# Performance work log

Hardware: AMD Instinct MI355X
Metric: run time of the kernel (lower is better)

## Reference

```python
import jax, jax.numpy as jnp
import numpy as np
import math

B, S, E, H = 4, 4096, 1024, 64

def setup_inputs() -> dict:
    key = jax.random.key(0)
    ks = jax.random.split(key, 4)
    scale = 1.0 / math.sqrt(E)
    return {
        "x": jax.random.normal(ks[0], (B, S, E), dtype=jnp.float32),
        "Wq": jax.random.normal(ks[1], (E, H), dtype=jnp.float32) * scale,
        "bq": jnp.zeros((H,), dtype=jnp.float32),
        "Wk": jax.random.normal(ks[2], (E, H), dtype=jnp.float32) * scale,
        "bk": jnp.zeros((H,), dtype=jnp.float32),
        "Wv": jax.random.normal(ks[3], (E, H), dtype=jnp.float32) * scale,
        "bv": jnp.zeros((H,), dtype=jnp.float32),
    }

def reference(x, Wq, bq, Wk, bk, Wv, bv):
    # x: [B,S,E]; single-head causal attention with dropout p=0 (eval).
    q = jnp.einsum("bse,eh->bsh", x, Wq) + bq  # [B,S,H]
    k = jnp.einsum("bse,eh->bsh", x, Wk) + bk
    v = jnp.einsum("bse,eh->bsh", x, Wv) + bv
    head_size = q.shape[-1]
    scores = jnp.einsum("bqh,bkh->bqk", q, k)  # [B,S,S]
    causal = jnp.tril(jnp.ones((q.shape[1], k.shape[1]), dtype=bool))
    # original: masked_fill(-inf) then divide by sqrt(head_size) -> same math
    scores = jnp.where(causal, scores, -jnp.inf) / jnp.sqrt(jnp.float32(head_size)).astype(scores.dtype)
    weight = jax.nn.softmax(scores, axis=-1)
    out = jnp.einsum("bqk,bkh->bqh", weight, v)  # [B,S,H]
    return out
```

## Files before the change

### kernel.cpp

```cpp
#include <hip/hip_runtime.h>

#define BATCH 4
#define SEQ   4096
#define EMB   1024
#define HD    64
#define NROW  (BATCH*SEQ)

typedef float f32x4  __attribute__((ext_vector_type(4)));
typedef short bf16x8 __attribute__((ext_vector_type(8)));
typedef short bf16x4 __attribute__((ext_vector_type(4)));

#define LOG2E 1.4426950408889634f
#define EXP2(x) exp2f(x)

static __device__ __forceinline__ f32x4 MFMA16(bf16x4 a, bf16x4 b, f32x4 c) {
#if defined(__HIP_DEVICE_COMPILE__) && __has_builtin(__builtin_amdgcn_mfma_f32_16x16x16bf16_1k)
  return __builtin_amdgcn_mfma_f32_16x16x16bf16_1k(a, b, c, 0, 0, 0);
#elif defined(__HIP_DEVICE_COMPILE__)
  f32x4 d;
  asm volatile("v_mfma_f32_16x16x16_bf16 %0, %1, %2, %3"
               : "=v"(d) : "v"(a), "v"(b), "v"(c));
  return d;
#else
  return c;
#endif
}

static __device__ __forceinline__ short f2bf(float f) {
  union { float f; unsigned u; } v; v.f = f;
  unsigned r = v.u + 0x7fffu + ((v.u >> 16) & 1u);
  return (short)(r >> 16);
}
static __device__ __forceinline__ float bf2f(short s) {
  union { unsigned u; float f; } v; v.u = ((unsigned)(unsigned short)s) << 16;
  return v.f;
}
static __device__ __forceinline__ unsigned cvtpk(float lo, float hi) {
  unsigned r;
  asm("v_cvt_pk_bf16_f32 %0, %1, %2" : "=v"(r) : "v"(lo), "v"(hi));
  return r;
}
static __device__ __forceinline__ float max3f(float a, float b, float c) {
  float r;
  asm("v_max3_f32 %0, %1, %2, %3" : "=v"(r) : "v"(a), "v"(b), "v"(c));
  return r;
}
static __device__ __forceinline__ bf16x4 pack4(unsigned w01, unsigned w23) {
  union { unsigned u[2]; bf16x4 v; } x;
  x.u[0] = w01; x.u[1] = w23;
  return x.v;
}

__global__ __launch_bounds__(256) void wt_kernel(
    const float* __restrict__ Wq, const float* __restrict__ Wk,
    const float* __restrict__ Wv, short* __restrict__ Wtf) {
  __shared__ float t[64][65];
  int bid = blockIdx.x;
  int mat = bid >> 4;
  int et  = bid & 15;
  int e0  = et * 64;
  const float* W = (mat == 0) ? Wq : (mat == 1) ? Wk : Wv;
  int c  = threadIdx.x & 63;
  int r0 = threadIdx.x >> 6;
#pragma unroll
  for (int i = 0; i < 16; ++i)
    t[i * 4 + r0][c] = W[(size_t)(e0 + i * 4 + r0) * HD + c];
  __syncthreads();
#pragma unroll
  for (int half = 0; half < 2; ++half) {
    int cid  = half * 256 + threadIdx.x;
    int ct4  = cid >> 7;
    int ksl  = (cid >> 6) & 1;
    int lane = cid & 63;
    int g    = lane >> 4;
    int mi   = lane & 15;
    int ct   = mat * 4 + ct4;
    int ks   = et * 2 + ksl;
    bf16x8 v;
#pragma unroll
    for (int j = 0; j < 8; ++j)
      v[j] = f2bf(t[ksl * 32 + 8 * g + j][ct4 * 16 + mi]);
    *(bf16x8*)(Wtf + ((size_t)(ct * 32 + ks) * 64 + lane) * 8) = v;
  }
}

__global__ __launch_bounds__(256) void qkv_kernel(
    const float* __restrict__ X, const short* __restrict__ Wtf,
    const float* __restrict__ bq, const float* __restrict__ bk, const float* __restrict__ bv,
    short* __restrict__ Qf, short* __restrict__ Kf, short* __restrict__ Vf) {
  __shared__ __align__(16) short xs[2][2][32][32];
  __shared__ float part[2][12][4][64];

  int tid  = threadIdx.x;
  int w    = tid >> 6;
  int lane = tid & 63;
  int g    = lane >> 4;
  int mi   = lane & 15;
  int rs   = w & 1;
  int h    = w >> 1;
  int rowbase = blockIdx.x * 32;

  int sr = tid >> 3;
  int sc = tid & 7;
  const float* xsrc = X + (size_t)(rowbase + sr) * EMB + sc * 4;

  f32x4 acc[12];
#pragma unroll
  for (int i = 0; i < 12; ++i) acc[i] = (f32x4){0.f, 0.f, 0.f, 0.f};

  {
    float4 xa = *(const float4*)(xsrc);
    float4 xb = *(const float4*)(xsrc + 512);
    bf16x4 va, vb;
    va[0] = f2bf(xa.x); va[1] = f2bf(xa.y); va[2] = f2bf(xa.z); va[3] = f2bf(xa.w);
    vb[0] = f2bf(xb.x); vb[1] = f2bf(xb.y); vb[2] = f2bf(xb.z); vb[3] = f2bf(xb.w);
    *(bf16x4*)(&xs[0][0][sr][sc * 4]) = va;
    *(bf16x4*)(&xs[0][1][sr][sc * 4]) = vb;
  }
  __syncthreads();

  const short* wp = Wtf + (size_t)(h * 16) * 512 + lane * 8;

#pragma unroll 2
  for (int ks = 0; ks < 16; ++ks) {
    int buf = ks & 1;
    float4 xa, xb;
    if (ks < 15) {
      xa = *(const float4*)(xsrc + (ks + 1) * 32);
      xb = *(const float4*)(xsrc + (ks + 1) * 32 + 512);
    }
    bf16x8 af = *(const bf16x8*)(&xs[buf][h][rs * 16 + mi][g * 8]);
    const short* wk = wp + ks * 512;
#pragma unroll
    for (int ct = 0; ct < 12; ++ct) {
      bf16x8 bfr = *(const bf16x8*)(wk + (size_t)ct * 16384);
      acc[ct] = __builtin_amdgcn_mfma_f32_16x16x32_bf16(af, bfr, acc[ct], 0, 0, 0);
    }
    if (ks < 15) {
      bf16x4 va, vb;
      va[0] = f2bf(xa.x); va[1] = f2bf(xa.y); va[2] = f2bf(xa.z); va[3] = f2bf(xa.w);
      vb[0] = f2bf(xb.x); vb[1] = f2bf(xb.y); vb[2] = f2bf(xb.z); vb[3] = f2bf(xb.w);
      *(bf16x4*)(&xs[buf ^ 1][0][sr][sc * 4]) = va;
      *(bf16x4*)(&xs[buf ^ 1][1][sr][sc * 4]) = vb;
    }
    __syncthreads();
  }

  if (h == 1) {
#pragma unroll
    for (int ct = 0; ct < 12; ++ct)
#pragma unroll
      for (int r = 0; r < 4; ++r) part[rs][ct][r][lane] = acc[ct][r];
  }
  __syncthreads();
  if (h == 0) {
#pragma unroll
    for (int ct = 0; ct < 12; ++ct)
#pragma unroll
      for (int r = 0; r < 4; ++r) part[rs][ct][r][lane] += acc[ct][r];
  }
  __syncthreads();

  int b_  = rowbase >> 12;
  int srb = rowbase & (SEQ - 1);

  {
    int tl  = tid >> 7;
    int kh  = (tid >> 6) & 1;
    int ln  = tid & 63;
    int gg  = ln >> 4;
    int mi2 = ln & 15;
    int tgl = (srb >> 4) + tl;
    bf16x8 vq, vk;
#pragma unroll
    for (int j = 0; j < 8; ++j) {
      int hd = kh * 32 + 8 * gg + j;
      int ct = hd >> 4, cc = hd & 15;
      int li = (mi2 >> 2) * 16 + cc;
      int r2 = mi2 & 3;
      vq[j] = f2bf(part[tl][ct][r2][li] + bq[hd]);
      vk[j] = f2bf(part[tl][4 + ct][r2][li] + bk[hd]);
    }
    size_t chunk = ((size_t)(b_ * 256 + tgl) * 2 + kh) * 512 + ln * 8;
    *(bf16x8*)(Qf + chunk) = vq;
    *(bf16x8*)(Kf + chunk) = vk;
  }
  {
    int ht  = tid >> 6;
    int ln  = tid & 63;
    int gg  = ln >> 4;
    int mi2 = ln & 15;
    int c32 = srb >> 5;
    float bias = bv[ht * 16 + mi2];
    bf16x8 vvv;
#pragma unroll
    for (int hl = 0; hl < 2; ++hl)
#pragma unroll
      for (int j = 0; j < 4; ++j)
        vvv[hl * 4 + j] = f2bf(part[hl][8 + ht][j][gg * 16 + mi2] + bias);
    size_t chunk = ((size_t)(b_ * 128 + c32) * 4 + ht) * 512 + ln * 8;
    *(bf16x8*)(Vf + chunk) = vvv;
  }
}

__global__ __launch_bounds__(512, 4) void attn_kernel(
    const short* __restrict__ Qf, const short* __restrict__ Kf,
    const short* __restrict__ Vf, float* __restrict__ out) {
  __shared__ short lds_o[8][64][17];
  __shared__ float lds_m[8][16];
  __shared__ float lds_l[8][16];

  int tid  = threadIdx.x;
  int w    = tid >> 6;
  int lane = tid & 63;
  int g    = lane >> 4;
  int qi   = lane & 15;

  int bid = blockIdx.x;
  int bb  = bid & 3;
  int jj  = (bid >> 3) + (((bid >> 2) & 1) << 6);

  const float K1 = 0.125f * LOG2E;

  for (int ph = 0; ph < 2; ++ph) {
    int t  = ph ? (255 - jj) : jj;
    int q0 = t * 16;
    int row = q0 + qi;

    const short* qp = Qf + ((size_t)(bb * 256 + t) * 2) * 512 + lane * 8;
    bf16x8 qf0 = *(const bf16x8*)(qp);
    bf16x8 qf1 = *(const bf16x8*)(qp + 512);

    int total64 = (t + 4) >> 2;
    int blo = (w * total64) >> 3;
    int bhi = ((w + 1) * total64) >> 3;

    float m2 = -INFINITY, lsum = 0.f;
    f32x4 o[4];
#pragma unroll
    for (int i = 0; i < 4; ++i) o[i] = (f32x4){0.f, 0.f, 0.f, 0.f};

    for (int b = blo; b < bhi; ++b) {
      int kv0 = b * 64;
      const short* kp = Kf + ((size_t)(bb * 256 + 4 * b) * 2) * 512 + lane * 8;
      const short* vp = Vf + ((size_t)(bb * 128 + 2 * b) * 4) * 512 + lane * 8;

      bf16x8 kfa[4], kfb[4];
#pragma unroll
      for (int c = 0; c < 4; ++c) {
        kfa[c] = *(const bf16x8*)(kp + (c * 2) * 512);
        kfb[c] = *(const bf16x8*)(kp + (c * 2 + 1) * 512);
      }
      bf16x8 vv[8];
#pragma unroll
      for (int i = 0; i < 8; ++i) vv[i] = *(const bf16x8*)(vp + i * 512);

      f32x4 z[4];
      __builtin_amdgcn_s_setprio(1);
#pragma unroll
      for (int c = 0; c < 4; ++c) {
        f32x4 zz = (f32x4){0.f, 0.f, 0.f, 0.f};
        zz = __builtin_amdgcn_mfma_f32_16x16x32_bf16(kfa[c], qf0, zz, 0, 0, 0);
        zz = __builtin_amdgcn_mfma_f32_16x16x32_bf16(kfb[c], qf1, zz, 0, 0, 0);
        z[c] = zz;
      }
      __builtin_amdgcn_s_setprio(0);

      if (kv0 + 63 > q0) {
#pragma unroll
        for (int c = 0; c < 4; ++c)
#pragma unroll
          for (int r = 0; r < 4; ++r) {
            int col = kv0 + c * 16 + 4 * g + r;
            z[c][r] = (col <= row) ? z[c][r] : -INFINITY;
          }
      }

      float l1 = max3f(z[0][0], z[0][1], z[0][2]);
      float l2 = max3f(z[0][3], z[1][0], z[1][1]);
      float l3 = max3f(z[1][2], z[1][3], z[2][0]);
      float l4 = max3f(z[2][1], z[2][2], z[2][3]);
      float l5 = max3f(z[3][0], z[3][1], z[3][2]);
      float lmax = fmaxf(max3f(l1, l2, l3), max3f(l4, l5, z[3][3]));
      bool grow = __any(fmaf(lmax, K1, -8.0f) > m2);
      if (grow) {
        float gm = fmaxf(lmax, __shfl_xor(lmax, 16));
        gm = fmaxf(gm, __shfl_xor(gm, 32));
        float m2n = fmaxf(m2, gm * K1);
        float alpha = EXP2(m2 - m2n);
        m2 = m2n;
        lsum *= alpha;
#pragma unroll
        for (int i = 0; i < 4; ++i) {
          o[i][0] *= alpha; o[i][1] *= alpha; o[i][2] *= alpha; o[i][3] *= alpha;
        }
      }

      float ls = 0.f;
      bf16x4 pb[4];
#pragma unroll
      for (int c = 0; c < 4; ++c) {
        float p0 = EXP2(fmaf(z[c][0], K1, -m2));
        float p1 = EXP2(fmaf(z[c][1], K1, -m2));
        float p2 = EXP2(fmaf(z[c][2], K1, -m2));
        float p3 = EXP2(fmaf(z[c][3], K1, -m2));
        ls += (p0 + p1) + (p2 + p3);
        pb[c] = pack4(cvtpk(p0, p1), cvtpk(p2, p3));
      }
      lsum += ls;

      __builtin_amdgcn_s_setprio(1);
#pragma unroll
      for (int c = 0; c < 4; ++c) {
        int h2 = c >> 1;
#pragma unroll
        for (int ht = 0; ht < 4; ++ht) {
          bf16x8 vfull = vv[h2 * 4 + ht];
          bf16x4 va = (c & 1) ? __builtin_shufflevector(vfull, vfull, 4, 5, 6, 7)
                              : __builtin_shufflevector(vfull, vfull, 0, 1, 2, 3);
          o[ht] = MFMA16(va, pb[c], o[ht]);
        }
      }
      __builtin_amdgcn_s_setprio(0);
    }

    lsum += __shfl_xor(lsum, 16);
    lsum += __shfl_xor(lsum, 32);
#pragma unroll
    for (int ht = 0; ht < 4; ++ht)
#pragma unroll
      for (int r = 0; r < 4; ++r)
        lds_o[w][ht * 16 + 4 * g + r][qi] = f2bf(o[ht][r]);
    if (lane < 16) { lds_m[w][lane] = m2; lds_l[w][lane] = lsum; }
    __syncthreads();

    {
      int q  = tid >> 5;
      int c2 = tid & 31;
      int hb = c2 * 2;
      float mm = lds_m[0][q];
#pragma unroll
      for (int wv = 1; wv < 8; ++wv) mm = fmaxf(mm, lds_m[wv][q]);
      float denom = 0.f, a0 = 0.f, a1 = 0.f;
#pragma unroll
      for (int wv = 0; wv < 8; ++wv) {
        float e = EXP2(lds_m[wv][q] - mm);
        denom += lds_l[wv][q] * e;
        a0 += e * bf2f(lds_o[wv][hb][q]);
        a1 += e * bf2f(lds_o[wv][hb + 1][q]);
      }
      float inv = 1.f / denom;
      float2 res = make_float2(a0 * inv, a1 * inv);
      *(float2*)(out + ((size_t)(bb * SEQ + q0 + q)) * HD + hb) = res;
    }
    __syncthreads();
  }
}

extern "C" void kernel_launch(void* const* d_in, const int* in_sizes, int n_in,
                              void* d_out, int out_size, void* d_ws, size_t ws_size,
                              hipStream_t stream) {
  const float* X  = (const float*)d_in[0];
  const float* Wq = (const float*)d_in[1];
  const float* bq = (const float*)d_in[2];
  const float* Wk = (const float*)d_in[3];
  const float* bk = (const float*)d_in[4];
  const float* Wv = (const float*)d_in[5];
  const float* bv = (const float*)d_in[6];
  float* out = (float*)d_out;

  char* ws = (char*)d_ws;
  const size_t SZ = (size_t)NROW * HD * 2;
  short* Qf  = (short*)(ws);
  short* Kf  = (short*)(ws + SZ);
  short* Vf  = (short*)(ws + 2 * SZ);
  short* Wtf = (short*)(ws + 3 * SZ);

  wt_kernel<<<48, 256, 0, stream>>>(Wq, Wk, Wv, Wtf);
  qkv_kernel<<<NROW / 32, 256, 0, stream>>>(X, Wtf, bq, bk, bv, Qf, Kf, Vf);
  attn_kernel<<<BATCH * 128, 512, 0, stream>>>(Qf, Kf, Vf, out);
}
```

Measured before the change: 56.47 us.

## Restructure QKV projection to 16-row blocks with full-K LDS staging

The QKV projection now processes 16 rows per block instead of 32. It loads the whole 16x1024 X tile into LDS as bf16 with an XOR swizzle, then splits the 12 output column tiles across the 4 waves (3 each). This removes the K-split partial-sum reduction and the per-step double-buffered syncs, and doubles the grid to raise parallelism in this memory-bound kernel. In exchange, each block re-reads the full weight matrix, so weight traffic from L2 per output row doubles, and the V output is written as half-chunk 8-byte stores.

Result: slower. 59.52 us (+5.4%).

```diff
diff --git a/kernel.cpp b/kernel.cpp
--- a/kernel.cpp
+++ b/kernel.cpp
@@ -84,122 +84,95 @@
   }
 }
 
-__global__ __launch_bounds__(256) void qkv_kernel(
+__global__ __launch_bounds__(256, 4) void qkv_kernel(
     const float* __restrict__ X, const short* __restrict__ Wtf,
     const float* __restrict__ bq, const float* __restrict__ bk, const float* __restrict__ bv,
     short* __restrict__ Qf, short* __restrict__ Kf, short* __restrict__ Vf) {
-  __shared__ __align__(16) short xs[2][2][32][32];
-  __shared__ float part[2][12][4][64];
+  __shared__ __align__(16) short xs[16384];
 
   int tid  = threadIdx.x;
   int w    = tid >> 6;
   int lane = tid & 63;
-  int g    = lane >> 4;
-  int mi   = lane & 15;
-  int rs   = w & 1;
-  int h    = w >> 1;
-  int rowbase = blockIdx.x * 32;
-
-  int sr = tid >> 3;
-  int sc = tid & 7;
-  const float* xsrc = X + (size_t)(rowbase + sr) * EMB + sc * 4;
-
-  f32x4 acc[12];
-#pragma unroll
-  for (int i = 0; i < 12; ++i) acc[i] = (f32x4){0.f, 0.f, 0.f, 0.f};
+  int rowbase = blockIdx.x * 16;
 
   {
-    float4 xa = *(const float4*)(xsrc);
-    float4 xb = *(const float4*)(xsrc + 512);
-    bf16x4 va, vb;
-    va[0] = f2bf(xa.x); va[1] = f2bf(xa.y); va[2] = f2bf(xa.z); va[3] = f2bf(xa.w);
-    vb[0] = f2bf(xb.x); vb[1] = f2bf(xb.y); vb[2] = f2bf(xb.z); vb[3] = f2bf(xb.w);
-    *(bf16x4*)(&xs[0][0][sr][sc * 4]) = va;
-    *(bf16x4*)(&xs[0][1][sr][sc * 4]) = vb;
+    int row = w * 4 + (lane >> 4);
+    int kb  = (lane & 15) * 4;
+    const float* xrow = X + (size_t)(rowbase + row) * EMB;
+#pragma unroll 4
+    for (int i = 0; i < 16; ++i) {
+      int k = i * 64 + kb;
+      float4 xv = *(const float4*)(xrow + k);
+      bf16x4 v;
+      v[0] = f2bf(xv.x); v[1] = f2bf(xv.y); v[2] = f2bf(xv.z); v[3] = f2bf(xv.w);
+      int ks = k >> 5, gg = (k >> 3) & 3, jh = (k >> 2) & 1;
+      int sidx = ks * 512 + ((((gg * 16 + row) * 8) ^ ((ks & 7) << 3)) + jh * 4);
+      *(bf16x4*)(&xs[sidx]) = v;
+    }
   }
   __syncthreads();
 
-  const short* wp = Wtf + (size_t)(h * 16) * 512 + lane * 8;
-
-#pragma unroll 2
-  for (int ks = 0; ks < 16; ++ks) {
-    int buf = ks & 1;
-    float4 xa, xb;
-    if (ks < 15) {
-      xa = *(const float4*)(xsrc + (ks + 1) * 32);
-      xb = *(const float4*)(xsrc + (ks + 1) * 32 + 512);
-    }
-    bf16x8 af = *(const bf16x8*)(&xs[buf][h][rs * 16 + mi][g * 8]);
-    const short* wk = wp + ks * 512;
-#pragma unroll
-    for (int ct = 0; ct < 12; ++ct) {
-      bf16x8 bfr = *(const bf16x8*)(wk + (size_t)ct * 16384);
-      acc[ct] = __builtin_amdgcn_mfma_f32_16x16x32_bf16(af, bfr, acc[ct], 0, 0, 0);
-    }
-    if (ks < 15) {
-      bf16x4 va, vb;
-      va[0] = f2bf(xa.x); va[1] = f2bf(xa.y); va[2] = f2bf(xa.z); va[3] = f2bf(xa.w);
-      vb[0] = f2bf(xb.x); vb[1] = f2bf(xb.y); vb[2] = f2bf(xb.z); vb[3] = f2bf(xb.w);
-      *(bf16x4*)(&xs[buf ^ 1][0][sr][sc * 4]) = va;
-      *(bf16x4*)(&xs[buf ^ 1][1][sr][sc * 4]) = vb;
-    }
-    __syncthreads();
-  }
-
-  if (h == 1) {
-#pragma unroll
-    for (int ct = 0; ct < 12; ++ct)
-#pragma unroll
-      for (int r = 0; r < 4; ++r) part[rs][ct][r][lane] = acc[ct][r];
+  f32x4 acc[3];
+#pragma unroll
+  for (int i = 0; i < 3; ++i) acc[i] = (f32x4){0.f, 0.f, 0.f, 0.f};
+  const short* wb = Wtf + ((size_t)(w * 3) * 32) * 512 + lane * 8;
+#pragma unroll 4
+  for (int ks = 0; ks < 32; ++ks) {
+    bf16x8 af = *(const bf16x8*)(&xs[ks * 512 + ((lane * 8) ^ ((ks & 7) << 3))]);
+#pragma unroll
+    for (int i = 0; i < 3; ++i) {
+      bf16x8 bfr = *(const bf16x8*)(wb + ((size_t)(i * 32 + ks)) * 512);
+      acc[i] = __builtin_amdgcn_mfma_f32_16x16x32_bf16(af, bfr, acc[i], 0, 0, 0);
+    }
   }
   __syncthreads();
-  if (h == 0) {
-#pragma unroll
-    for (int ct = 0; ct < 12; ++ct)
-#pragma unroll
-      for (int r = 0; r < 4; ++r) part[rs][ct][r][lane] += acc[ct][r];
+
+  float* part = (float*)xs;
+#pragma unroll
+  for (int i = 0; i < 3; ++i) {
+    int ct = w * 3 + i;
+#pragma unroll
+    for (int r = 0; r < 4; ++r) part[(ct * 4 + r) * 64 + lane] = acc[i][r];
   }
   __syncthreads();
 
   int b_  = rowbase >> 12;
   int srb = rowbase & (SEQ - 1);
+  int tgl = srb >> 4;
+  int c32 = srb >> 5;
+  int hl  = (srb >> 4) & 1;
 
   {
-    int tl  = tid >> 7;
+    int qk  = tid >> 7;
     int kh  = (tid >> 6) & 1;
     int ln  = tid & 63;
     int gg  = ln >> 4;
     int mi2 = ln & 15;
-    int tgl = (srb >> 4) + tl;
-    bf16x8 vq, vk;
+    const float* bp = qk ? bk : bq;
+    bf16x8 v;
 #pragma unroll
     for (int j = 0; j < 8; ++j) {
       int hd = kh * 32 + 8 * gg + j;
-      int ct = hd >> 4, cc = hd & 15;
+      int ct = qk * 4 + (hd >> 4);
+      int cc = hd & 15;
       int li = (mi2 >> 2) * 16 + cc;
       int r2 = mi2 & 3;
-      vq[j] = f2bf(part[tl][ct][r2][li] + bq[hd]);
-      vk[j] = f2bf(part[tl][4 + ct][r2][li] + bk[hd]);
+      v[j] = f2bf(part[(ct * 4 + r2) * 64 + li] + bp[hd]);
     }
     size_t chunk = ((size_t)(b_ * 256 + tgl) * 2 + kh) * 512 + ln * 8;
-    *(bf16x8*)(Qf + chunk) = vq;
-    *(bf16x8*)(Kf + chunk) = vk;
+    *(bf16x8*)((qk ? Kf : Qf) + chunk) = v;
   }
   {
     int ht  = tid >> 6;
     int ln  = tid & 63;
     int gg  = ln >> 4;
     int mi2 = ln & 15;
-    int c32 = srb >> 5;
     float bias = bv[ht * 16 + mi2];
-    bf16x8 vvv;
-#pragma unroll
-    for (int hl = 0; hl < 2; ++hl)
-#pragma unroll
-      for (int j = 0; j < 4; ++j)
-        vvv[hl * 4 + j] = f2bf(part[hl][8 + ht][j][gg * 16 + mi2] + bias);
-    size_t chunk = ((size_t)(b_ * 128 + c32) * 4 + ht) * 512 + ln * 8;
-    *(bf16x8*)(Vf + chunk) = vvv;
+    bf16x4 vv;
+#pragma unroll
+    for (int j = 0; j < 4; ++j)
+      vv[j] = f2bf(part[((8 + ht) * 4 + j) * 64 + gg * 16 + mi2] + bias);
+    *(bf16x4*)(Vf + ((size_t)(b_ * 128 + c32) * 4 + ht) * 512 + ln * 8 + hl * 4) = vv;
   }
 }
 
@@ -377,6 +350,6 @@
   short* Wtf = (short*)(ws + 3 * SZ);
 
   wt_kernel<<<48, 256, 0, stream>>>(Wq, Wk, Wv, Wtf);
-  qkv_kernel<<<NROW / 32, 256, 0, stream>>>(X, Wtf, bq, bk, bv, Qf, Kf, Vf);
+  qkv_kernel<<<NROW / 16, 256, 0, stream>>>(X, Wtf, bq, bk, bv, Qf, Kf, Vf);
   attn_kernel<<<BATCH * 128, 512, 0, stream>>>(Qf, Kf, Vf, out);
 }
```

## Process two query tiles per block to reuse K/V loads across 32 rows

Applied to the files above, without the earlier changes.

Each attention block now computes two 16-row query tiles per phase, sharing each loaded K and V tile across both, and the grid is halved to 256 blocks. This is meant to cut redundant K/V global loads and raise MFMA work per load. In exchange it doubles accumulator registers, lowers launch-bounds occupancy to 2, and leaves only one block per CU, reducing latency hiding and load balance.

Result: no change. 56.47 us, median of 3 (-0.0%).

```diff
diff --git a/kernel.cpp b/kernel.cpp
--- a/kernel.cpp
+++ b/kernel.cpp
@@ -203,12 +203,12 @@
   }
 }
 
-__global__ __launch_bounds__(512, 4) void attn_kernel(
+__global__ __launch_bounds__(512, 2) void attn_kernel(
     const short* __restrict__ Qf, const short* __restrict__ Kf,
     const short* __restrict__ Vf, float* __restrict__ out) {
-  __shared__ short lds_o[8][64][17];
-  __shared__ float lds_m[8][16];
-  __shared__ float lds_l[8][16];
+  __shared__ short lds_o[8][2][64][17];
+  __shared__ float lds_m[8][2][16];
+  __shared__ float lds_l[8][2][16];
 
   int tid  = threadIdx.x;
   int w    = tid >> 6;
@@ -218,27 +218,33 @@
 
   int bid = blockIdx.x;
   int bb  = bid & 3;
-  int jj  = (bid >> 3) + (((bid >> 2) & 1) << 6);
+  int j   = bid >> 2;
 
   const float K1 = 0.125f * LOG2E;
 
   for (int ph = 0; ph < 2; ++ph) {
-    int t  = ph ? (255 - jj) : jj;
-    int q0 = t * 16;
-    int row = q0 + qi;
-
-    const short* qp = Qf + ((size_t)(bb * 256 + t) * 2) * 512 + lane * 8;
-    bf16x8 qf0 = *(const bf16x8*)(qp);
-    bf16x8 qf1 = *(const bf16x8*)(qp + 512);
-
-    int total64 = (t + 4) >> 2;
+    int G  = ph ? (127 - j) : j;
+    int q0 = G * 32;
+
+    bf16x8 qf0[2], qf1[2];
+#pragma unroll
+    for (int tl = 0; tl < 2; ++tl) {
+      const short* qp = Qf + ((size_t)(bb * 256 + 2 * G + tl) * 2) * 512 + lane * 8;
+      qf0[tl] = *(const bf16x8*)(qp);
+      qf1[tl] = *(const bf16x8*)(qp + 512);
+    }
+
+    int total64 = (G + 2) >> 1;
     int blo = (w * total64) >> 3;
     int bhi = ((w + 1) * total64) >> 3;
 
-    float m2 = -INFINITY, lsum = 0.f;
-    f32x4 o[4];
-#pragma unroll
-    for (int i = 0; i < 4; ++i) o[i] = (f32x4){0.f, 0.f, 0.f, 0.f};
+    float m2[2]   = {-INFINITY, -INFINITY};
+    float lsum[2] = {0.f, 0.f};
+    f32x4 o[2][4];
+#pragma unroll
+    for (int tl = 0; tl < 2; ++tl)
+#pragma unroll
+      for (int i = 0; i < 4; ++i) o[tl][i] = (f32x4){0.f, 0.f, 0.f, 0.f};
 
     for (int b = blo; b < bhi; ++b) {
       int kv0 = b * 64;
@@ -255,103 +261,119 @@
 #pragma unroll
       for (int i = 0; i < 8; ++i) vv[i] = *(const bf16x8*)(vp + i * 512);
 
-      f32x4 z[4];
+      f32x4 z[2][4];
       __builtin_amdgcn_s_setprio(1);
 #pragma unroll
-      for (int c = 0; c < 4; ++c) {
-        f32x4 zz = (f32x4){0.f, 0.f, 0.f, 0.f};
-        zz = __builtin_amdgcn_mfma_f32_16x16x32_bf16(kfa[c], qf0, zz, 0, 0, 0);
-        zz = __builtin_amdgcn_mfma_f32_16x16x32_bf16(kfb[c], qf1, zz, 0, 0, 0);
-        z[c] = zz;
-      }
+      for (int tl = 0; tl < 2; ++tl)
+#pragma unroll
+        for (int c = 0; c < 4; ++c) {
+          f32x4 zz = (f32x4){0.f, 0.f, 0.f, 0.f};
+          zz = __builtin_amdgcn_mfma_f32_16x16x32_bf16(kfa[c], qf0[tl], zz, 0, 0, 0);
+          zz = __builtin_amdgcn_mfma_f32_16x16x32_bf16(kfb[c], qf1[tl], zz, 0, 0, 0);
+          z[tl][c] = zz;
+        }
       __builtin_amdgcn_s_setprio(0);
 
       if (kv0 + 63 > q0) {
 #pragma unroll
-        for (int c = 0; c < 4; ++c)
-#pragma unroll
-          for (int r = 0; r < 4; ++r) {
-            int col = kv0 + c * 16 + 4 * g + r;
-            z[c][r] = (col <= row) ? z[c][r] : -INFINITY;
-          }
-      }
-
-      float l1 = max3f(z[0][0], z[0][1], z[0][2]);
-      float l2 = max3f(z[0][3], z[1][0], z[1][1]);
-      float l3 = max3f(z[1][2], z[1][3], z[2][0]);
-      float l4 = max3f(z[2][1], z[2][2], z[2][3]);
-      float l5 = max3f(z[3][0], z[3][1], z[3][2]);
-      float lmax = fmaxf(max3f(l1, l2, l3), max3f(l4, l5, z[3][3]));
-      bool grow = __any(fmaf(lmax, K1, -8.0f) > m2);
-      if (grow) {
-        float gm = fmaxf(lmax, __shfl_xor(lmax, 16));
-        gm = fmaxf(gm, __shfl_xor(gm, 32));
-        float m2n = fmaxf(m2, gm * K1);
-        float alpha = EXP2(m2 - m2n);
-        m2 = m2n;
-        lsum *= alpha;
-#pragma unroll
-        for (int i = 0; i < 4; ++i) {
-          o[i][0] *= alpha; o[i][1] *= alpha; o[i][2] *= alpha; o[i][3] *= alpha;
+        for (int tl = 0; tl < 2; ++tl) {
+          int rowt = q0 + tl * 16 + qi;
+#pragma unroll
+          for (int c = 0; c < 4; ++c)
+#pragma unroll
+            for (int r = 0; r < 4; ++r) {
+              int col = kv0 + c * 16 + 4 * g + r;
+              z[tl][c][r] = (col <= rowt) ? z[tl][c][r] : -INFINITY;
+            }
         }
       }
 
-      float ls = 0.f;
-      bf16x4 pb[4];
-#pragma unroll
-      for (int c = 0; c < 4; ++c) {
-        float p0 = EXP2(fmaf(z[c][0], K1, -m2));
-        float p1 = EXP2(fmaf(z[c][1], K1, -m2));
-        float p2 = EXP2(fmaf(z[c][2], K1, -m2));
-        float p3 = EXP2(fmaf(z[c][3], K1, -m2));
-        ls += (p0 + p1) + (p2 + p3);
-        pb[c] = pack4(cvtpk(p0, p1), cvtpk(p2, p3));
+      bf16x4 pb[2][4];
+#pragma unroll
+      for (int tl = 0; tl < 2; ++tl) {
+        float l1 = max3f(z[tl][0][0], z[tl][0][1], z[tl][0][2]);
+        float l2 = max3f(z[tl][0][3], z[tl][1][0], z[tl][1][1]);
+        float l3 = max3f(z[tl][1][2], z[tl][1][3], z[tl][2][0]);
+        float l4 = max3f(z[tl][2][1], z[tl][2][2], z[tl][2][3]);
+        float l5 = max3f(z[tl][3][0], z[tl][3][1], z[tl][3][2]);
+        float lmax = fmaxf(max3f(l1, l2, l3), max3f(l4, l5, z[tl][3][3]));
+        bool grow = __any(fmaf(lmax, K1, -8.0f) > m2[tl]);
+        if (grow) {
+          float gm = fmaxf(lmax, __shfl_xor(lmax, 16));
+          gm = fmaxf(gm, __shfl_xor(gm, 32));
+          float m2n = fmaxf(m2[tl], gm * K1);
+          float alpha = EXP2(m2[tl] - m2n);
+          m2[tl] = m2n;
+          lsum[tl] *= alpha;
+#pragma unroll
+          for (int i = 0; i < 4; ++i) {
+            o[tl][i][0] *= alpha; o[tl][i][1] *= alpha;
+            o[tl][i][2] *= alpha; o[tl][i][3] *= alpha;
+          }
+        }
+        float ls = 0.f;
+#pragma unroll
+        for (int c = 0; c < 4; ++c) {
+          float p0 = EXP2(fmaf(z[tl][c][0], K1, -m2[tl]));
+          float p1 = EXP2(fmaf(z[tl][c][1], K1, -m2[tl]));
+          float p2 = EXP2(fmaf(z[tl][c][2], K1, -m2[tl]));
+          float p3 = EXP2(fmaf(z[tl][c][3], K1, -m2[tl]));
+          ls += (p0 + p1) + (p2 + p3);
+          pb[tl][c] = pack4(cvtpk(p0, p1), cvtpk(p2, p3));
+        }
+        lsum[tl] += ls;
       }
-      lsum += ls;
 
       __builtin_amdgcn_s_setprio(1);
 #pragma unroll
-      for (int c = 0; c < 4; ++c) {
-        int h2 = c >> 1;
-#pragma unroll
-        for (int ht = 0; ht < 4; ++ht) {
-          bf16x8 vfull = vv[h2 * 4 + ht];
-          bf16x4 va = (c & 1) ? __builtin_shufflevector(vfull, vfull, 4, 5, 6, 7)
-                              : __builtin_shufflevector(vfull, vfull, 0, 1, 2, 3);
-          o[ht] = MFMA16(va, pb[c], o[ht]);
+      for (int tl = 0; tl < 2; ++tl)
+#pragma unroll
+        for (int c = 0; c < 4; ++c) {
+          int h2 = c >> 1;
+#pragma unroll
+          for (int ht = 0; ht < 4; ++ht) {
+            bf16x8 vfull = vv[h2 * 4 + ht];
+            bf16x4 va = (c & 1) ? __builtin_shufflevector(vfull, vfull, 4, 5, 6, 7)
+                                : __builtin_shufflevector(vfull, vfull, 0, 1, 2, 3);
+            o[tl][ht] = MFMA16(va, pb[tl][c], o[tl][ht]);
+          }
         }
-      }
       __builtin_amdgcn_s_setprio(0);
     }
 
-    lsum += __shfl_xor(lsum, 16);
-    lsum += __shfl_xor(lsum, 32);
-#pragma unroll
-    for (int ht = 0; ht < 4; ++ht)
-#pragma unroll
-      for (int r = 0; r < 4; ++r)
-        lds_o[w][ht * 16 + 4 * g + r][qi] = f2bf(o[ht][r]);
-    if (lane < 16) { lds_m[w][lane] = m2; lds_l[w][lane] = lsum; }
+#pragma unroll
+    for (int tl = 0; tl < 2; ++tl) {
+      float ls = lsum[tl];
+      ls += __shfl_xor(ls, 16);
+      ls += __shfl_xor(ls, 32);
+#pragma unroll
+      for (int ht = 0; ht < 4; ++ht)
+#pragma unroll
+        for (int r = 0; r < 4; ++r)
+          lds_o[w][tl][ht * 16 + 4 * g + r][qi] = f2bf(o[tl][ht][r]);
+      if (lane < 16) { lds_m[w][tl][lane] = m2[tl]; lds_l[w][tl][lane] = ls; }
+    }
     __syncthreads();
 
-    {
+#pragma unroll
+    for (int tl = 0; tl < 2; ++tl) {
       int q  = tid >> 5;
       int c2 = tid & 31;
       int hb = c2 * 2;
-      float mm = lds_m[0][q];
-#pragma unroll
-      for (int wv = 1; wv < 8; ++wv) mm = fmaxf(mm, lds_m[wv][q]);
+      float mm = lds_m[0][tl][q];
+#pragma unroll
+      for (int wv = 1; wv < 8; ++wv) mm = fmaxf(mm, lds_m[wv][tl][q]);
       float denom = 0.f, a0 = 0.f, a1 = 0.f;
 #pragma unroll
       for (int wv = 0; wv < 8; ++wv) {
-        float e = EXP2(lds_m[wv][q] - mm);
-        denom += lds_l[wv][q] * e;
-        a0 += e * bf2f(lds_o[wv][hb][q]);
-        a1 += e * bf2f(lds_o[wv][hb + 1][q]);
+        float e = EXP2(lds_m[wv][tl][q] - mm);
+        denom += lds_l[wv][tl][q] * e;
+        a0 += e * bf2f(lds_o[wv][tl][hb][q]);
+        a1 += e * bf2f(lds_o[wv][tl][hb + 1][q]);
       }
       float inv = 1.f / denom;
       float2 res = make_float2(a0 * inv, a1 * inv);
-      *(float2*)(out + ((size_t)(bb * SEQ + q0 + q)) * HD + hb) = res;
+      *(float2*)(out + ((size_t)(bb * SEQ + q0 + tl * 16 + q)) * HD + hb) = res;
     }
     __syncthreads();
   }
@@ -378,5 +400,5 @@
 
   wt_kernel<<<48, 256, 0, stream>>>(Wq, Wk, Wv, Wtf);
   qkv_kernel<<<NROW / 32, 256, 0, stream>>>(X, Wtf, bq, bk, bv, Qf, Kf, Vf);
-  attn_kernel<<<BATCH * 128, 512, 0, stream>>>(Qf, Kf, Vf, out);
-}
+  attn_kernel<<<256, 512, 0, stream>>>(Qf, Kf, Vf, out);
+}
```
